# Kernel tuning notes

Measured on AMD Instinct MI355X. Metric: run time of the kernel, lower is better.

The kernel has to match this reference:

```python
import jax, jax.numpy as jnp
import numpy as np

W_L2 = 1.0      # cfg['topological']['w_l2']
W_TOPO = 0.1    # cfg['topological']['w_topo']
BATCH_SIZE = 16 # cfg['batch_size']
EPS = 1e-12


def _pairwise_dist(x):
    # x: [N, D] -> [N, N] Euclidean distances, diagonal set to +inf
    sq = jnp.sum(x * x, axis=-1)
    d2 = sq[:, None] + sq[None, :] - 2.0 * (x @ x.T)
    d2 = jnp.maximum(d2, 0.0)
    N = x.shape[0]
    d2 = jnp.where(jnp.eye(N, dtype=bool), jnp.inf, d2)
    return jnp.sqrt(d2 + EPS)


def _h0_deaths(D):
    # H0 Vietoris-Rips persistence: finite bars are (0, w) for each MST edge
    # weight w. Vectorized Prim's algorithm via lax.scan (N-1 steps).
    N = D.shape[0]
    in_tree = jnp.zeros((N,), dtype=bool).at[0].set(True)
    mind = D[0].at[0].set(jnp.inf)  # min distance from tree to each node

    def step(carry, _):
        mind, in_tree = carry
        i = jnp.argmin(mind)
        w = mind[i]                       # MST edge weight = H0 death time
        in_tree = in_tree.at[i].set(True)
        mind = jnp.where(in_tree, jnp.inf, jnp.minimum(mind, D[i]))
        return (mind, in_tree), w

    _, deaths = jax.lax.scan(step, (mind, in_tree), None, length=N - 1)
    return deaths  # [N-1]


def _wasserstein_p2(d1, d2):
    # Persistence diagrams here are {(0, death)}: births all zero, equal
    # cardinality -> optimal p=2 matching pairs sorted death times.
    s1 = jnp.sort(d1)
    s2 = jnp.sort(d2)
    return jnp.sqrt(jnp.sum((s1 - s2) ** 2))


def reference(x_1, x_2):
    # MSE representation loss
    representation_loss = jnp.mean((x_1 - x_2) ** 2)

    # VR H0 persistence diagrams per batch element
    deaths_fn = jax.vmap(lambda x: _h0_deaths(_pairwise_dist(x)))
    d1 = deaths_fn(x_1)  # [B, N-1]
    d2 = deaths_fn(x_2)  # [B, N-1]

    w12 = jnp.mean(jax.vmap(_wasserstein_p2)(d1, d2))
    w21 = jnp.mean(jax.vmap(_wasserstein_p2)(d2, d1))
    topological_loss = (w12 + w21) / 2.0 * BATCH_SIZE

    return W_L2 * representation_loss + W_TOPO * topological_loss


def setup_inputs() -> dict:
    key = jax.random.key(0)
    k1, k2 = jax.random.split(key)
    B, N, D = 16, 1024, 128
    x_1 = jax.random.normal(k1, (B, N, D), dtype=jnp.float32)
    x_2 = jax.random.normal(k2, (B, N, D), dtype=jnp.float32)
    return {"x_1": x_1, "x_2": x_2}
```

## Files before the change

### kernel.cpp

```cpp
#include <hip/hip_runtime.h>
#include <hip/hip_fp16.h>
#include <math.h>

#define NPTS 1024
#define DIM  128
#define BATCH 16
#define NCLOUD 32
#define BIGF 3.0e38f
#define BMAX 0xFFFFFFFFFFFFFFFFull

#define DEATHS_OFF 64
#define D_OFF 196608
#define XBF_OFF ((size_t)D_OFF + (size_t)NCLOUD * NPTS * NPTS * 2)
#define SQ_OFF   (XBF_OFF + (size_t)NCLOUD * NPTS * DIM * 2)
#define BEST_OFF (SQ_OFF + (size_t)NCLOUD * NPTS * 4)
#define CAND_OFF (BEST_OFF + (size_t)NCLOUD * NPTS * 8)
#define WS_NEED  (CAND_OFF + (size_t)NCLOUD * NPTS * 16 * 8)

typedef __attribute__((ext_vector_type(8))) short short8;
typedef __attribute__((ext_vector_type(4))) float f32x4;

__device__ __forceinline__ unsigned umin32(unsigned a, unsigned b) { return a < b ? a : b; }
__device__ __forceinline__ unsigned umax32(unsigned a, unsigned b) { return a > b ? a : b; }

__device__ __forceinline__ unsigned bfbits(float f) {
  unsigned u = __float_as_uint(f);
  return (u + 0x7FFFu + ((u >> 16) & 1u)) >> 16;
}

__global__ __launch_bounds__(256) void prep_mse(const float* __restrict__ x1,
                                                const float* __restrict__ x2,
                                                unsigned short* __restrict__ xbf,
                                                float* __restrict__ sqg,
                                                unsigned long long* __restrict__ best,
                                                double* __restrict__ acc) {
  const int b = blockIdx.x;
  const int s = blockIdx.y;
  const int tid = threadIdx.x;

  const int half = tid >> 7;
  const int r = s * 128 + (tid & 127);
  const int cloud = half * 16 + b;
  const float* xc = (half ? x2 : x1) + (size_t)b * NPTS * DIM;
  const float4* xr = (const float4*)(xc + (size_t)r * DIM);
  const float4* yr = (const float4*)(x2 + (size_t)b * NPTS * DIM + (size_t)r * DIM);
  uint4* orow = (uint4*)xbf + (size_t)cloud * NPTS * (DIM / 8) + (size_t)r * (DIM / 8);

  float mse_s = 0.f;
  float ax = 0.f, ay = 0.f, az = 0.f, aw = 0.f;
  #pragma unroll 4
  for (int m = 0; m < 32; m += 2) {
    float4 v0 = xr[m], v1 = xr[m + 1];
    ax = fmaf(v0.x, v0.x, ax); ay = fmaf(v0.y, v0.y, ay);
    az = fmaf(v0.z, v0.z, az); aw = fmaf(v0.w, v0.w, aw);
    ax = fmaf(v1.x, v1.x, ax); ay = fmaf(v1.y, v1.y, ay);
    az = fmaf(v1.z, v1.z, az); aw = fmaf(v1.w, v1.w, aw);
    uint4 o;
    o.x = bfbits(v0.x) | (bfbits(v0.y) << 16);
    o.y = bfbits(v0.z) | (bfbits(v0.w) << 16);
    o.z = bfbits(v1.x) | (bfbits(v1.y) << 16);
    o.w = bfbits(v1.z) | (bfbits(v1.w) << 16);
    orow[m >> 1] = o;
    if (half == 0) {
      float4 u0 = yr[m], u1 = yr[m + 1];
      float d0 = v0.x - u0.x, d1 = v0.y - u0.y, d2 = v0.z - u0.z, d3 = v0.w - u0.w;
      float e0 = v1.x - u1.x, e1 = v1.y - u1.y, e2 = v1.z - u1.z, e3 = v1.w - u1.w;
      mse_s += d0 * d0 + d1 * d1 + d2 * d2 + d3 * d3;
      mse_s += e0 * e0 + e1 * e1 + e2 * e2 + e3 * e3;
    }
  }
  sqg[cloud * NPTS + r] = (ax + ay) + (az + aw);
  best[cloud * NPTS + r] = BMAX;

  #pragma unroll
  for (int off = 32; off; off >>= 1) mse_s += __shfl_xor(mse_s, off);
  __shared__ float wsum[4];
  int lane = tid & 63, wid = tid >> 6;
  if (lane == 0) wsum[wid] = mse_s;
  __syncthreads();
  if (tid == 0)
    atomicAdd(acc, (double)(wsum[0] + wsum[1] + wsum[2] + wsum[3]));
}

__global__ __launch_bounds__(256) void distmat_mfma(const unsigned short* __restrict__ xbf,
                                                    const float* __restrict__ sqg,
                                                    unsigned short* __restrict__ Dmat,
                                                    unsigned long long* __restrict__ best,
                                                    uint2* __restrict__ cand) {
  const int cloud = blockIdx.z;
  const int i0 = blockIdx.y * 64;
  const int j0 = blockIdx.x * 64;
  const int tid = threadIdx.x;
  const int lane = tid & 63, w = tid >> 6;
  const int l15 = lane & 15, kq = lane >> 4;

  __shared__ unsigned short Ash[64 * 128];
  __shared__ unsigned short Bsh[64 * 128];
  __shared__ float sqi_sh[64], sqj_sh[64];

  const uint4* xg = (const uint4*)xbf + (size_t)cloud * NPTS * (DIM / 8);
  uint4* A4 = (uint4*)Ash;
  uint4* B4 = (uint4*)Bsh;

  #pragma unroll
  for (int c = tid; c < 1024; c += 256) {
    int row = c >> 4, c16 = c & 15;
    int sidx = (row << 4) | (c16 ^ (row & 7));
    A4[sidx] = xg[((size_t)(i0 + row) << 4) | c16];
    B4[sidx] = xg[((size_t)(j0 + row) << 4) | c16];
  }
  if (tid < 64) sqi_sh[tid] = sqg[(size_t)cloud * NPTS + i0 + tid];
  else if (tid < 128) sqj_sh[tid - 64] = sqg[(size_t)cloud * NPTS + j0 + tid - 64];
  __syncthreads();

  const int ar = w * 16 + l15;
  f32x4 acc[4];
  #pragma unroll
  for (int jt = 0; jt < 4; ++jt) acc[jt] = (f32x4){0.f, 0.f, 0.f, 0.f};

  #pragma unroll
  for (int kk = 0; kk < 4; ++kk) {
    int acol = (kk * 4 + kq) ^ (ar & 7);
    short8 a = *(const short8*)&A4[(ar << 4) | acol];
    #pragma unroll
    for (int jt = 0; jt < 4; ++jt) {
      int br = jt * 16 + l15;
      int bcol = (kk * 4 + kq) ^ (br & 7);
      short8 bf = *(const short8*)&B4[(br << 4) | bcol];
      acc[jt] = __builtin_amdgcn_mfma_f32_16x16x32_bf16(a, bf, acc[jt], 0, 0, 0);
    }
  }

  unsigned short* Dc = Dmat + ((size_t)cloud << 20);
  unsigned long long* bestc = best + cloud * NPTS;

  unsigned k1[4] = {0xFFFFFFFFu, 0xFFFFFFFFu, 0xFFFFFFFFu, 0xFFFFFFFFu};
  unsigned k2[4] = {0xFFFFFFFFu, 0xFFFFFFFFu, 0xFFFFFFFFu, 0xFFFFFFFFu};

  #pragma unroll
  for (int jt = 0; jt < 4; ++jt) {
    int jl = jt * 16 + l15;
    int gj = j0 + jl;
    float sqj = sqj_sh[jl];
    #pragma unroll
    for (int r = 0; r < 4; ++r) {
      int il = w * 16 + kq * 4 + r;
      int gi = i0 + il;
      float d2 = sqi_sh[il] + sqj - 2.f * acc[jt][r];
      float d = sqrtf(fmaxf(d2, 0.f) + 1e-12f);
      unsigned h = (gi == gj) ? 0x7C00u : (unsigned)__half_as_ushort(__float2half(d));
      Dc[(size_t)gi * NPTS + gj] = (unsigned short)h;
      unsigned key = (h << 16) | (unsigned)gj;
      if (key < k1[r]) { k2[r] = k1[r]; k1[r] = key; }
      else if (key < k2[r]) k2[r] = key;
    }
  }

  #pragma unroll
  for (int mask = 1; mask < 16; mask <<= 1) {
    #pragma unroll
    for (int r = 0; r < 4; ++r) {
      unsigned o1 = __shfl_xor(k1[r], mask);
      unsigned o2 = __shfl_xor(k2[r], mask);
      unsigned n1 = umin32(k1[r], o1);
      unsigned n2 = umin32(umax32(k1[r], o1), umin32(k2[r], o2));
      k1[r] = n1; k2[r] = n2;
    }
  }

  if (l15 == 0) {
    #pragma unroll
    for (int r = 0; r < 4; ++r) {
      unsigned gi = (unsigned)(i0 + w * 16 + kq * 4 + r);
      cand[(((size_t)(cloud * 16 + blockIdx.x)) << 10) + gi] = make_uint2(k1[r], k2[r]);
      unsigned j = k1[r] & 0xFFFFu, hv = k1[r] >> 16;
      unsigned cmn = umin32(gi, j);
      unsigned cmx = gi + j - cmn;
      unsigned long long k64 =
          ((unsigned long long)hv << 20) | (unsigned long long)((cmn << 10) | cmx);
      atomicMin(&bestc[gi], k64);
    }
  }
}

__global__ __launch_bounds__(1024) void boruvka_solve(const unsigned short* __restrict__ Dmat,
                                                      const uint2* __restrict__ cand,
                                                      const unsigned long long* __restrict__ best_init,
                                                      float* __restrict__ deaths_out) {
  const int cloud = blockIdx.x;
  const int tid = threadIdx.x;
  const int lane = tid & 63, wid = tid >> 6;

  __shared__ unsigned short comp16[NPTS];
  __shared__ unsigned short par[NPTS];
  __shared__ unsigned long long best64[NPTS];
  __shared__ float dl[NPTS];
  __shared__ unsigned short fb[NPTS];
  __shared__ unsigned nfb_sh, dcnt_sh;

  uint2 c[16];
  const uint2* candc = cand + ((size_t)cloud << 14);
  #pragma unroll
  for (int s = 0; s < 16; ++s) c[s] = candc[(s << 10) + tid];

  comp16[tid] = (unsigned short)tid;
  par[tid] = (unsigned short)tid;
  best64[tid] = best_init[cloud * NPTS + tid];
  dl[tid] = BIGF;
  if (tid == 0) { dcnt_sh = 0; nfb_sh = 0; }
  __syncthreads();

  const uint4* p = (const uint4*)(Dmat + ((size_t)cloud << 20));
  const unsigned jb0 = (unsigned)(lane << 3), jb1 = 512u + jb0;

  for (int rnd = 0; rnd < 11; ++rnd) {
    if (rnd > 0) {
      unsigned ci = comp16[tid];
      unsigned e = 0xFFFFFFFFu;
      unsigned bw = 0xFFFFu;
      #pragma unroll
      for (int s = 0; s < 16; ++s) {
        unsigned j1 = c[s].x & 0xFFFFu, j2 = c[s].y & 0xFFFFu;
        bool o1 = ((unsigned)comp16[j1] != ci);
        bool o2 = ((unsigned)comp16[j2] != ci);
        unsigned es = o1 ? c[s].x : (o2 ? c[s].y : 0xFFFFFFFFu);
        unsigned bs = (!o1 && !o2) ? (c[s].y >> 16) : 0xFFFFu;
        e = umin32(e, es);
        bw = umin32(bw, bs);
      }
      if (e != 0xFFFFFFFFu) {
        unsigned j = e & 0xFFFFu, hv = e >> 16;
        unsigned cmn = umin32((unsigned)tid, j);
        unsigned cmx = (unsigned)tid + j - cmn;
        unsigned long long k64 =
            ((unsigned long long)hv << 20) | (unsigned long long)((cmn << 10) | cmx);
        atomicMin(&best64[ci], k64);
      }
      __syncthreads();

      unsigned bestw = (unsigned)((best64[ci] >> 20) & 0xFFFFu);
      if (bw <= bestw) {
        unsigned slot = atomicAdd(&nfb_sh, 1u);
        fb[slot] = (unsigned short)tid;
      }
      __syncthreads();

      unsigned nfb = nfb_sh;
      if (nfb) {
        unsigned cj[16];
        #pragma unroll
        for (int q = 0; q < 8; ++q) cj[q] = comp16[jb0 + q];
        #pragma unroll
        for (int q = 0; q < 8; ++q) cj[8 + q] = comp16[jb1 + q];
        for (unsigned k = (unsigned)wid; k < nfb; k += 16) {
          int frow = fb[k];
          unsigned fci = (unsigned)comp16[frow];
          uint4 ra = p[frow * 128 + lane];
          uint4 rb = p[frow * 128 + 64 + lane];
          unsigned key = 0xFFFFFFFFu;
          #define ENT(word, cl, ch, jb) { \
            unsigned klo = ((word) << 16) | (jb); \
            unsigned khi = ((word) & 0xFFFF0000u) | ((jb) + 1); \
            key = umin32(key, (cl) == fci ? 0xFFFFFFFFu : klo); \
            key = umin32(key, (ch) == fci ? 0xFFFFFFFFu : khi); }
          ENT(ra.x, cj[0],  cj[1],  jb0 + 0) ENT(ra.y, cj[2],  cj[3],  jb0 + 2)
          ENT(ra.z, cj[4],  cj[5],  jb0 + 4) ENT(ra.w, cj[6],  cj[7],  jb0 + 6)
          ENT(rb.x, cj[8],  cj[9],  jb1 + 0) ENT(rb.y, cj[10], cj[11], jb1 + 2)
          ENT(rb.z, cj[12], cj[13], jb1 + 4) ENT(rb.w, cj[14], cj[15], jb1 + 6)
          #undef ENT
          #define DPPMIN(ctrl) { \
            unsigned tv = (unsigned)__builtin_amdgcn_update_dpp((int)key, (int)key, (ctrl), 0xF, 0xF, false); \
            key = umin32(key, tv); }
          DPPMIN(0x111) DPPMIN(0x112) DPPMIN(0x114) DPPMIN(0x118)
          DPPMIN(0x142) DPPMIN(0x143)
          #undef DPPMIN
          if (lane == 63 && key != 0xFFFFFFFFu) {
            unsigned wv = key >> 16, v = key & 0xFFFFu;
            unsigned cmn = umin32((unsigned)frow, v);
            unsigned cmx = (unsigned)frow + v - cmn;
            unsigned long long k64 =
                ((unsigned long long)wv << 20) | (unsigned long long)((cmn << 10) | cmx);
            atomicMin(&best64[fci], k64);
          }
        }
        __syncthreads();
      }
    }

    unsigned long long bk = best64[tid];
    unsigned cold = comp16[tid];
    unsigned partner = (unsigned)tid;
    unsigned wb = 0;
    if (cold == (unsigned)tid && bk != BMAX) {
      wb = (unsigned)(bk >> 20) & 0xFFFFu;
      unsigned cmin = (unsigned)(bk >> 10) & 1023u;
      unsigned cmax = (unsigned)bk & 1023u;
      unsigned ca = comp16[cmin], cb = comp16[cmax];
      partner = (ca == (unsigned)tid) ? cb : ca;
      par[tid] = (unsigned short)partner;
    }
    __syncthreads();
    unsigned pp = par[partner];
    bool twoc = (partner != (unsigned)tid) && (pp == (unsigned)tid);
    bool winner = twoc && ((unsigned)tid < partner);
    bool append = (partner != (unsigned)tid) && !winner;
    __syncthreads();
    if (winner) par[tid] = (unsigned short)tid;
    if (append) {
      unsigned slot = atomicAdd(&dcnt_sh, 1u);
      dl[slot] = __half2float(__ushort_as_half((unsigned short)wb));
    }
    __syncthreads();
    if (dcnt_sh == NPTS - 1) break;

    unsigned x = cold;
    unsigned px = par[x];
    while (px != x) { x = px; px = par[x]; }
    __syncthreads();
    comp16[tid] = (unsigned short)x;
    par[tid] = (unsigned short)tid;
    best64[tid] = BMAX;
    if (tid == 0) nfb_sh = 0;
    __syncthreads();
  }
  __syncthreads();

  float v = dl[tid];
  for (int k = 2; k <= NPTS; k <<= 1) {
    bool up = ((tid & k) == 0);
    for (int jj = k >> 1; jj > 0; jj >>= 1) {
      float pv;
      if (jj >= 64) {
        __syncthreads();
        dl[tid] = v;
        __syncthreads();
        pv = dl[tid ^ jj];
      } else {
        pv = __shfl_xor(v, jj);
      }
      bool lower = ((tid & jj) == 0);
      v = (lower == up) ? fminf(v, pv) : fmaxf(v, pv);
    }
  }
  deaths_out[(size_t)cloud * NPTS + tid] = v;
}

__global__ __launch_bounds__(256) void mse_kernel(const float* __restrict__ a,
                                                  const float* __restrict__ b,
                                                  double* __restrict__ acc, int n4) {
  int i = blockIdx.x * blockDim.x + threadIdx.x;
  int stride = gridDim.x * blockDim.x;
  const float4* a4 = (const float4*)a;
  const float4* b4 = (const float4*)b;
  float s = 0.f;
  for (int k = i; k < n4; k += stride) {
    float4 va = a4[k], vb = b4[k];
    float dx = va.x - vb.x, dy = va.y - vb.y, dz = va.z - vb.z, dw = va.w - vb.w;
    s += dx * dx + dy * dy + dz * dz + dw * dw;
  }
  #pragma unroll
  for (int off = 32; off; off >>= 1) s += __shfl_xor(s, off);
  __shared__ float wsum[4];
  int lane = threadIdx.x & 63, wid = threadIdx.x >> 6;
  if (lane == 0) wsum[wid] = s;
  __syncthreads();
  if (threadIdx.x == 0)
    atomicAdd(acc, (double)(wsum[0] + wsum[1] + wsum[2] + wsum[3]));
}

__global__ __launch_bounds__(1024) void prim_kernel(const float* __restrict__ x1,
                                                    const float* __restrict__ x2,
                                                    float* __restrict__ sorted_out) {
  const int cloud = blockIdx.x;
  const int b = cloud & (BATCH - 1);
  const int src = cloud >> 4;
  const float* xbase = (src ? x2 : x1) + (size_t)b * NPTS * DIM;
  const int j = threadIdx.x;

  __shared__ float xi_sh[DIM];
  __shared__ float sq_sh[NPTS];
  __shared__ float redw[16];
  __shared__ int   redi[16];
  __shared__ float deaths[NPTS];

  const float4* xr = (const float4*)(xbase + (size_t)j * DIM);
  {
    float ax = 0.f, ay = 0.f, az = 0.f, aw = 0.f;
    #pragma unroll 8
    for (int m = 0; m < DIM / 4; ++m) {
      float4 v = xr[m];
      ax = fmaf(v.x, v.x, ax); ay = fmaf(v.y, v.y, ay);
      az = fmaf(v.z, v.z, az); aw = fmaf(v.w, v.w, aw);
    }
    sq_sh[j] = (ax + ay) + (az + aw);
  }
  const float sqj = sq_sh[j];

  float mind = BIGF;
  bool in_tree = (j == 0);
  int  cur = 0;

  for (int t = 0; t < NPTS - 1; ++t) {
    if (threadIdx.x < DIM / 4)
      ((float4*)xi_sh)[threadIdx.x] = ((const float4*)(xbase + (size_t)cur * DIM))[threadIdx.x];
    __syncthreads();

    const float4* xi4 = (const float4*)xi_sh;
    float ax = 0.f, ay = 0.f, az = 0.f, aw = 0.f;
    #pragma unroll 8
    for (int m = 0; m < DIM / 4; ++m) {
      float4 v = xr[m];
      float4 u = xi4[m];
      ax = fmaf(v.x, u.x, ax); ay = fmaf(v.y, u.y, ay);
      az = fmaf(v.z, u.z, az); aw = fmaf(v.w, u.w, aw);
    }
    float dot = (ax + ay) + (az + aw);
    float d2 = sq_sh[cur] + sqj - 2.f * dot;
    float d = sqrtf(fmaxf(d2, 0.f) + 1e-12f);
    mind = in_tree ? BIGF : fminf(mind, d);

    float w = mind;
    int idx = j;
    #pragma unroll
    for (int off = 32; off; off >>= 1) {
      float w2 = __shfl_xor(w, off);
      int i2 = __shfl_xor(idx, off);
      if (w2 < w || (w2 == w && i2 < idx)) { w = w2; idx = i2; }
    }
    int lane = j & 63, wid = j >> 6;
    if (lane == 0) { redw[wid] = w; redi[wid] = idx; }
    __syncthreads();

    float cw = redw[0];
    int ci = redi[0];
    #pragma unroll
    for (int q = 1; q < 16; ++q) {
      float w2 = redw[q]; int i2 = redi[q];
      if (w2 < cw || (w2 == cw && i2 < ci)) { cw = w2; ci = i2; }
    }
    if (j == ci) in_tree = true;
    if (j == 0)  deaths[t] = cw;
    cur = ci;
  }

  if (threadIdx.x == 0) deaths[NPTS - 1] = BIGF;
  __syncthreads();

  for (int k = 2; k <= NPTS; k <<= 1) {
    for (int jj = k >> 1; jj > 0; jj >>= 1) {
      int i = threadIdx.x;
      int l = i ^ jj;
      if (l > i) {
        float va = deaths[i], vb = deaths[l];
        bool up = ((i & k) == 0);
        if ((va > vb) == up) { deaths[i] = vb; deaths[l] = va; }
      }
      __syncthreads();
    }
  }
  sorted_out[(size_t)cloud * NPTS + threadIdx.x] = deaths[threadIdx.x];
}

__global__ __launch_bounds__(1024) void final_kernel(const double* __restrict__ mse_acc,
                                                     const float* __restrict__ sorted,
                                                     float* __restrict__ out) {
  int wid = threadIdx.x >> 6;
  int lane = threadIdx.x & 63;
  const float* s1 = sorted + (size_t)wid * NPTS;
  const float* s2 = sorted + (size_t)(BATCH + wid) * NPTS;
  float s = 0.f;
  for (int k = lane; k < NPTS; k += 64) {
    float dlt = s1[k] - s2[k];
    s += dlt * dlt;
  }
  #pragma unroll
  for (int off = 32; off; off >>= 1) s += __shfl_xor(s, off);
  __shared__ float part[16];
  if (lane == 0) part[wid] = sqrtf(s);
  __syncthreads();
  if (threadIdx.x == 0) {
    float topo = 0.f;
    #pragma unroll
    for (int q = 0; q < 16; ++q) topo += part[q];
    float mse = (float)(mse_acc[0] / (double)((size_t)BATCH * NPTS * DIM));
    out[0] = 1.0f * mse + 0.1f * topo;
  }
}

extern "C" void kernel_launch(void* const* d_in, const int* in_sizes, int n_in,
                              void* d_out, int out_size, void* d_ws, size_t ws_size,
                              hipStream_t stream) {
  const float* x1 = (const float*)d_in[0];
  const float* x2 = (const float*)d_in[1];
  double* mse_acc = (double*)d_ws;
  float* deaths   = (float*)((char*)d_ws + DEATHS_OFF);
  float* out      = (float*)d_out;

  hipMemsetAsync(d_ws, 0, 64, stream);

  if (ws_size >= WS_NEED) {
    unsigned short* Dmat = (unsigned short*)((char*)d_ws + D_OFF);
    unsigned short* xbf  = (unsigned short*)((char*)d_ws + XBF_OFF);
    float* sqg           = (float*)((char*)d_ws + SQ_OFF);
    unsigned long long* best = (unsigned long long*)((char*)d_ws + BEST_OFF);
    uint2* cand          = (uint2*)((char*)d_ws + CAND_OFF);

    prep_mse<<<dim3(BATCH, 8), 256, 0, stream>>>(x1, x2, xbf, sqg, best, mse_acc);
    distmat_mfma<<<dim3(16, 16, NCLOUD), 256, 0, stream>>>(xbf, sqg, Dmat, best, cand);
    boruvka_solve<<<NCLOUD, 1024, 0, stream>>>(Dmat, cand, best, deaths);
  } else {
    int n4 = (BATCH * NPTS * DIM) / 4;
    mse_kernel<<<1024, 256, 0, stream>>>(x1, x2, mse_acc, n4);
    prim_kernel<<<NCLOUD, 1024, 0, stream>>>(x1, x2, deaths);
  }

  final_kernel<<<1, 1024, 0, stream>>>(mse_acc, deaths, out);
}
```

Before: 101.1 us.

## Exploit distance-matrix symmetry: compute only lower-triangular tiles and mirror results

The distance kernel now launches 136 lower-triangular 64x64 tiles per cloud instead of all 256, mapping a linear block index to (by,bx) via a triangular-number inverse. Each off-diagonal tile writes its transposed block into the matrix and also computes per-column top-2 candidates, reduced via shuffles and shared memory, to fill the mirrored candidate and best entries. This roughly halves the MFMA and load work, at the cost of strided transposed stores, an extra reduction, a barrier and extra atomics per tile.

```diff
diff --git a/kernel.cpp b/kernel.cpp
--- a/kernel.cpp
+++ b/kernel.cpp
@@ -87,9 +87,18 @@
                                                     unsigned short* __restrict__ Dmat,
                                                     unsigned long long* __restrict__ best,
                                                     uint2* __restrict__ cand) {
-  const int cloud = blockIdx.z;
-  const int i0 = blockIdx.y * 64;
-  const int j0 = blockIdx.x * 64;
+  const int cloud = blockIdx.y;
+  {
+  }
+  int t = blockIdx.x;
+  int by = (int)((sqrtf(8.f * (float)t + 1.f) - 1.f) * 0.5f);
+  while ((by + 1) * (by + 2) / 2 <= t) ++by;
+  while (by * (by + 1) / 2 > t) --by;
+  const int bx = t - by * (by + 1) / 2;
+  const int i0 = by * 64;
+  const int j0 = bx * 64;
+  const bool diag = (bx == by);
+
   const int tid = threadIdx.x;
   const int lane = tid & 63, w = tid >> 6;
   const int l15 = lane & 15, kq = lane >> 4;
@@ -97,6 +106,7 @@
   __shared__ unsigned short Ash[64 * 128];
   __shared__ unsigned short Bsh[64 * 128];
   __shared__ float sqi_sh[64], sqj_sh[64];
+  __shared__ uint2 colred[4][4][16];
 
   const uint4* xg = (const uint4*)xbf + (size_t)cloud * NPTS * (DIM / 8);
   uint4* A4 = (uint4*)Ash;
@@ -134,14 +144,19 @@
   unsigned short* Dc = Dmat + ((size_t)cloud << 20);
   unsigned long long* bestc = best + cloud * NPTS;
 
-  unsigned k1[4] = {0xFFFFFFFFu, 0xFFFFFFFFu, 0xFFFFFFFFu, 0xFFFFFFFFu};
-  unsigned k2[4] = {0xFFFFFFFFu, 0xFFFFFFFFu, 0xFFFFFFFFu, 0xFFFFFFFFu};
+  unsigned k1[4]  = {0xFFFFFFFFu, 0xFFFFFFFFu, 0xFFFFFFFFu, 0xFFFFFFFFu};
+  unsigned k2[4]  = {0xFFFFFFFFu, 0xFFFFFFFFu, 0xFFFFFFFFu, 0xFFFFFFFFu};
+  unsigned ck1[4] = {0xFFFFFFFFu, 0xFFFFFFFFu, 0xFFFFFFFFu, 0xFFFFFFFFu};
+  unsigned ck2[4] = {0xFFFFFFFFu, 0xFFFFFFFFu, 0xFFFFFFFFu, 0xFFFFFFFFu};
+
+  const int gib = i0 + w * 16 + kq * 4;
 
   #pragma unroll
   for (int jt = 0; jt < 4; ++jt) {
     int jl = jt * 16 + l15;
     int gj = j0 + jl;
     float sqj = sqj_sh[jl];
+    unsigned hh[4];
     #pragma unroll
     for (int r = 0; r < 4; ++r) {
       int il = w * 16 + kq * 4 + r;
@@ -149,10 +164,18 @@
       float d2 = sqi_sh[il] + sqj - 2.f * acc[jt][r];
       float d = sqrtf(fmaxf(d2, 0.f) + 1e-12f);
       unsigned h = (gi == gj) ? 0x7C00u : (unsigned)__half_as_ushort(__float2half(d));
+      hh[r] = h;
       Dc[(size_t)gi * NPTS + gj] = (unsigned short)h;
-      unsigned key = (h << 16) | (unsigned)gj;
-      if (key < k1[r]) { k2[r] = k1[r]; k1[r] = key; }
-      else if (key < k2[r]) k2[r] = key;
+      unsigned rkey = (h << 16) | (unsigned)gj;
+      if (rkey < k1[r]) { k2[r] = k1[r]; k1[r] = rkey; }
+      else if (rkey < k2[r]) k2[r] = rkey;
+      unsigned ckey = (h << 16) | (unsigned)gi;
+      if (ckey < ck1[jt]) { ck2[jt] = ck1[jt]; ck1[jt] = ckey; }
+      else if (ckey < ck2[jt]) ck2[jt] = ckey;
+    }
+    if (!diag) {
+      *(uint2*)&Dc[((size_t)gj << 10) + gib] =
+          make_uint2(hh[0] | (hh[1] << 16), hh[2] | (hh[3] << 16));
     }
   }
 
@@ -167,18 +190,57 @@
       k1[r] = n1; k2[r] = n2;
     }
   }
-
   if (l15 == 0) {
     #pragma unroll
     for (int r = 0; r < 4; ++r) {
-      unsigned gi = (unsigned)(i0 + w * 16 + kq * 4 + r);
-      cand[(((size_t)(cloud * 16 + blockIdx.x)) << 10) + gi] = make_uint2(k1[r], k2[r]);
+      unsigned gi = (unsigned)(gib + r);
+      cand[(((size_t)(cloud * 16 + bx)) << 10) + gi] = make_uint2(k1[r], k2[r]);
       unsigned j = k1[r] & 0xFFFFu, hv = k1[r] >> 16;
       unsigned cmn = umin32(gi, j);
       unsigned cmx = gi + j - cmn;
       unsigned long long k64 =
           ((unsigned long long)hv << 20) | (unsigned long long)((cmn << 10) | cmx);
       atomicMin(&bestc[gi], k64);
+    }
+  }
+
+  if (!diag) {
+    #pragma unroll
+    for (int mask = 16; mask < 64; mask <<= 1) {
+      #pragma unroll
+      for (int jt = 0; jt < 4; ++jt) {
+        unsigned o1 = __shfl_xor(ck1[jt], mask);
+        unsigned o2 = __shfl_xor(ck2[jt], mask);
+        unsigned n1 = umin32(ck1[jt], o1);
+        unsigned n2 = umin32(umax32(ck1[jt], o1), umin32(ck2[jt], o2));
+        ck1[jt] = n1; ck2[jt] = n2;
+      }
+    }
+    if (lane < 16) {
+      #pragma unroll
+      for (int jt = 0; jt < 4; ++jt) colred[w][jt][l15] = make_uint2(ck1[jt], ck2[jt]);
+    }
+    __syncthreads();
+    if (tid < 64) {
+      int c = tid;
+      int jt = c >> 4, li = c & 15;
+      uint2 a0 = colred[0][jt][li], a1 = colred[1][jt][li];
+      uint2 a2 = colred[2][jt][li], a3 = colred[3][jt][li];
+      unsigned m1 = a0.x, m2 = a0.y;
+      #define MRG(v) { unsigned b1 = (v).x, b2 = (v).y; \
+        unsigned n1 = umin32(m1, b1); \
+        unsigned n2 = umin32(umax32(m1, b1), umin32(m2, b2)); \
+        m1 = n1; m2 = n2; }
+      MRG(a1) MRG(a2) MRG(a3)
+      #undef MRG
+      unsigned gj = (unsigned)(j0 + c);
+      cand[(((size_t)(cloud * 16 + by)) << 10) + gj] = make_uint2(m1, m2);
+      unsigned j = m1 & 0xFFFFu, hv = m1 >> 16;
+      unsigned cmn = umin32(gj, j);
+      unsigned cmx = gj + j - cmn;
+      unsigned long long k64 =
+          ((unsigned long long)hv << 20) | (unsigned long long)((cmn << 10) | cmx);
+      atomicMin(&bestc[gj], k64);
     }
   }
 }
@@ -506,7 +568,7 @@
     uint2* cand          = (uint2*)((char*)d_ws + CAND_OFF);
 
     prep_mse<<<dim3(BATCH, 8), 256, 0, stream>>>(x1, x2, xbf, sqg, best, mse_acc);
-    distmat_mfma<<<dim3(16, 16, NCLOUD), 256, 0, stream>>>(xbf, sqg, Dmat, best, cand);
+    distmat_mfma<<<dim3(136, NCLOUD), 256, 0, stream>>>(xbf, sqg, Dmat, best, cand);
     boruvka_solve<<<NCLOUD, 1024, 0, stream>>>(Dmat, cand, best, deaths);
   } else {
     int n4 = (BATCH * NPTS * DIM) / 4;
```

New measurement: 87.59 us. -13.4%, faster.
